# Kernel tuning notes

Measured on AMD Instinct MI355X. Metric: run time of the kernel, lower is better.

Reference implementation:

```python
import jax, jax.numpy as jnp
import numpy as np

N_NODES = 20000
N_EDGES = 320000
N_FEAT = 128
HID = 64
HEADS = 4
N_CLS = 16
NEG_SLOPE = 0.2


def setup_inputs() -> dict:
    key = jax.random.key(0)
    ks = jax.random.split(key, 12)
    x = jax.random.normal(ks[0], (N_NODES, N_FEAT), dtype=jnp.float32)
    edge_index = jax.random.randint(ks[1], (2, N_EDGES), 0, N_NODES, dtype=jnp.int64)
    # layer 1: GATConv(128 -> 64, heads=4, concat)
    s1 = 1.0 / np.sqrt(N_FEAT)
    W1 = jax.random.uniform(ks[2], (N_FEAT, HEADS * HID), jnp.float32, -s1, s1)
    a_src1 = jax.random.uniform(ks[3], (HEADS, HID), jnp.float32, -s1, s1)
    a_dst1 = jax.random.uniform(ks[4], (HEADS, HID), jnp.float32, -s1, s1)
    b1 = jnp.zeros((HEADS * HID,), jnp.float32)
    # layer 2: GATConv(256 -> 16, heads=1)
    s2 = 1.0 / np.sqrt(HEADS * HID)
    W2 = jax.random.uniform(ks[5], (HEADS * HID, N_CLS), jnp.float32, -s2, s2)
    a_src2 = jax.random.uniform(ks[6], (1, N_CLS), jnp.float32, -s2, s2)
    a_dst2 = jax.random.uniform(ks[7], (1, N_CLS), jnp.float32, -s2, s2)
    b2 = jnp.zeros((N_CLS,), jnp.float32)
    return {"x": x, "edge_index": edge_index, "W1": W1, "a_src1": a_src1,
            "a_dst1": a_dst1, "b1": b1, "W2": W2, "a_src2": a_src2,
            "a_dst2": a_dst2, "b2": b2}


def gat_conv(x, src, dst, W, a_src, a_dst, bias, n_nodes):
    # x: [N, F_in]; W: [F_in, H*C]; a_src/a_dst: [H, C]
    H, C = a_src.shape
    h = (x @ W).reshape(n_nodes, H, C)                     # [N, H, C]
    al_src = jnp.sum(h * a_src[None], axis=-1)             # [N, H]
    al_dst = jnp.sum(h * a_dst[None], axis=-1)             # [N, H]
    e = jax.nn.leaky_relu(al_src[src] + al_dst[dst], NEG_SLOPE)  # [E, H]
    # segment softmax over incoming edges of each destination node
    m = jax.ops.segment_max(e, dst, num_segments=n_nodes)  # [N, H]
    e = jnp.exp(e - m[dst])
    denom = jax.ops.segment_sum(e, dst, num_segments=n_nodes)
    alpha = e / (denom[dst] + 1e-16)                       # [E, H]
    msg = h[src] * alpha[:, :, None]                       # [E, H, C]
    out = jax.ops.segment_sum(msg, dst, num_segments=n_nodes)  # [N, H, C]
    return out.reshape(n_nodes, H * C) + bias


def reference(x, edge_index, W1, a_src1, a_dst1, b1, W2, a_src2, a_dst2, b2):
    n = x.shape[0]
    loops = jnp.arange(n, dtype=edge_index.dtype)
    src = jnp.concatenate([edge_index[0], loops])
    dst = jnp.concatenate([edge_index[1], loops])
    # eval mode: dropout is identity
    h = jax.nn.elu(gat_conv(x, src, dst, W1, a_src1, a_dst1, b1, n))
    out = gat_conv(h, src, dst, W2, a_src2, a_dst2, b2, n)
    return out
```

## Files before the change

### kernel.cpp

```cpp
#include <hip/hip_runtime.h>
#include <hip/hip_bf16.h>
#include <hip/hip_fp16.h>
#include <math.h>

#define N_NODES 20000
#define N_EDGES 320000
#define E_TOT   (N_EDGES + N_NODES)
#define N_FEAT  128
#define NEG_SLOPE 0.2f
#define MAXDEG  96

typedef _Float16 half8 __attribute__((ext_vector_type(8)));
typedef float f32x4 __attribute__((ext_vector_type(4)));

__global__ void k_zero(int* __restrict__ cur){
  int i = blockIdx.x * blockDim.x + threadIdx.x;
  if (i < N_NODES) cur[i] = 0;
}

__global__ void k_pre(const int* __restrict__ ei, int* __restrict__ cur,
                      int* __restrict__ adjS,
                      const float* __restrict__ x, _Float16* __restrict__ xh,
                      const float* __restrict__ W1, _Float16* __restrict__ W1t){
  int tid = blockIdx.x * blockDim.x + threadIdx.x;
  if (tid < E_TOT){
    int s, d;
    if (tid < N_EDGES){ s = ei[tid]; d = ei[N_EDGES + tid]; }
    else              { s = d = tid - N_EDGES; }
    int pos = atomicAdd(&cur[d], 1);
    if (pos < MAXDEG) adjS[d * MAXDEG + pos] = s;
  }
  if (tid < (N_NODES * N_FEAT / 8)){
    float4 a = *(const float4*)&x[(size_t)tid * 8];
    float4 b = *(const float4*)&x[(size_t)tid * 8 + 4];
    union { __half2 h2[4]; half8 h8; } u;
    u.h2[0] = __floats2half2_rn(a.x, a.y);
    u.h2[1] = __floats2half2_rn(a.z, a.w);
    u.h2[2] = __floats2half2_rn(b.x, b.y);
    u.h2[3] = __floats2half2_rn(b.z, b.w);
    *(half8*)&xh[(size_t)tid * 8] = u.h8;
  }
  int u2 = tid - (N_NODES * N_FEAT / 8);
  if (u2 >= 0 && u2 < 4096){
    int n = u2 >> 4, ks = u2 & 15;
    union { __half2 h2[4]; half8 h8; } u;
    float v[8];
    #pragma unroll
    for (int r = 0; r < 8; ++r) v[r] = W1[(size_t)(ks * 8 + r) * 256 + n];
    u.h2[0] = __floats2half2_rn(v[0], v[1]);
    u.h2[1] = __floats2half2_rn(v[2], v[3]);
    u.h2[2] = __floats2half2_rn(v[4], v[5]);
    u.h2[3] = __floats2half2_rn(v[6], v[7]);
    *(half8*)&W1t[(size_t)n * 128 + ks * 8] = u.h8;
  }
}

__global__ __launch_bounds__(256) void k_gemm1(
                        const _Float16* __restrict__ xh, const _Float16* __restrict__ W1t,
                        const float* __restrict__ as1, const float* __restrict__ ad1,
                        _Float16* __restrict__ h1h,
                        float* __restrict__ alS, float* __restrict__ alD){
  __shared__ _Float16 xt[64][136];
  __shared__ _Float16 Wt[64][136];
  int t  = threadIdx.x;
  int m0 = blockIdx.x * 64;
  int by = blockIdx.y;
  int j0 = by * 64;
  #pragma unroll
  for (int ii = 0; ii < 4; ++ii){
    int f = t + ii * 256;
    int r = f >> 4, s = f & 15;
    half8 xv = (half8)(_Float16)0.f;
    if (m0 + r < N_NODES) xv = *(const half8*)&xh[(size_t)(m0 + r) * 128 + s * 8];
    *(half8*)&xt[r][s * 8] = xv;
    half8 wv = *(const half8*)&W1t[(size_t)(j0 + r) * 128 + s * 8];
    *(half8*)&Wt[r][s * 8] = wv;
  }
  __syncthreads();

  int w = t >> 6, lane = t & 63;
  int g = lane >> 4, mi = lane & 15;
  f32x4 acc[4] = {};
  #pragma unroll
  for (int kk = 0; kk < 4; ++kk){
    int ko = kk * 32 + g * 8;
    half8 b = *(const half8*)&xt[w * 16 + mi][ko];
    #pragma unroll
    for (int s = 0; s < 4; ++s){
      half8 a = *(const half8*)&Wt[s * 16 + mi][ko];
      acc[s] = __builtin_amdgcn_mfma_f32_16x16x32_f16(a, b, acc[s], 0, 0, 0);
    }
  }

  int m = m0 + w * 16 + mi;
  float s_ = 0.f, d_ = 0.f;
  #pragma unroll
  for (int s = 0; s < 4; ++s){
    int nb = j0 + s * 16 + g * 4;
    float4 asv = *(const float4*)&as1[nb];
    float4 adv = *(const float4*)&ad1[nb];
    s_ += acc[s][0] * asv.x + acc[s][1] * asv.y + acc[s][2] * asv.z + acc[s][3] * asv.w;
    d_ += acc[s][0] * adv.x + acc[s][1] * adv.y + acc[s][2] * adv.z + acc[s][3] * adv.w;
    if (m < N_NODES){
      union { __half2 h2[2]; float2 f2; } u;
      u.h2[0] = __floats2half2_rn(acc[s][0], acc[s][1]);
      u.h2[1] = __floats2half2_rn(acc[s][2], acc[s][3]);
      *(float2*)&h1h[(size_t)m * 256 + nb] = u.f2;
    }
  }
  s_ += __shfl_xor(s_, 16); s_ += __shfl_xor(s_, 32);
  d_ += __shfl_xor(d_, 16); d_ += __shfl_xor(d_, 32);
  if (g == 0 && m < N_NODES){ alS[m * 4 + by] = s_; alD[m * 4 + by] = d_; }
}

__global__ __launch_bounds__(256) void k_attn1(
                        const int* __restrict__ cur, const int* __restrict__ adjS,
                        const __half* __restrict__ h1h,
                        const float* __restrict__ alS, const float* __restrict__ alD,
                        const float* __restrict__ b1, float* __restrict__ helu){
  int b    = blockIdx.x;
  int slot = b & 7;
  int h    = slot & 3;
  int g    = (slot >> 2) * 625 + (b >> 3);
  int t    = threadIdx.x;
  int w    = t >> 6, lane = t & 63;
  int grp  = lane >> 4, l16 = lane & 15;
  int n    = g * 16 + w * 4 + grp;

  int cnt  = cur[n]; cnt = (cnt > MAXDEG) ? MAXDEG : cnt;
  int start = n * MAXDEG, end = start + cnt;
  float ald = alD[n * 4 + h];
  const __half* __restrict__ hb = h1h + h * 64 + l16 * 4;

  float4 A0 = make_float4(0.f,0.f,0.f,0.f), A1 = A0, A2 = A0, A3 = A0;
  float d0 = 0.f, d1 = 0.f, d2 = 0.f, d3 = 0.f;
  int i = start;
  for (; i + 3 < end; i += 4){
    int s0 = adjS[i],     s1 = adjS[i + 1];
    int s2 = adjS[i + 2], s3 = adjS[i + 3];
    float t0 = alS[s0 * 4 + h] + ald;
    float t1 = alS[s1 * 4 + h] + ald;
    float t2 = alS[s2 * 4 + h] + ald;
    float t3 = alS[s3 * 4 + h] + ald;
    t0 = (t0 > 0.f) ? t0 : NEG_SLOPE * t0;
    t1 = (t1 > 0.f) ? t1 : NEG_SLOPE * t1;
    t2 = (t2 > 0.f) ? t2 : NEG_SLOPE * t2;
    t3 = (t3 > 0.f) ? t3 : NEG_SLOPE * t3;
    float w0 = __expf(t0), w1 = __expf(t1), w2 = __expf(t2), w3 = __expf(t3);
    float2 r0 = *(const float2*)&hb[(size_t)s0 * 256];
    float2 r1 = *(const float2*)&hb[(size_t)s1 * 256];
    float2 r2 = *(const float2*)&hb[(size_t)s2 * 256];
    float2 r3 = *(const float2*)&hb[(size_t)s3 * 256];
    const __half2* p0 = (const __half2*)&r0;
    const __half2* p1 = (const __half2*)&r1;
    const __half2* p2 = (const __half2*)&r2;
    const __half2* p3 = (const __half2*)&r3;
    float2 v0a = __half22float2(p0[0]), v0b = __half22float2(p0[1]);
    float2 v1a = __half22float2(p1[0]), v1b = __half22float2(p1[1]);
    float2 v2a = __half22float2(p2[0]), v2b = __half22float2(p2[1]);
    float2 v3a = __half22float2(p3[0]), v3b = __half22float2(p3[1]);
    A0.x += w0 * v0a.x; A0.y += w0 * v0a.y; A0.z += w0 * v0b.x; A0.w += w0 * v0b.y;
    A1.x += w1 * v1a.x; A1.y += w1 * v1a.y; A1.z += w1 * v1b.x; A1.w += w1 * v1b.y;
    A2.x += w2 * v2a.x; A2.y += w2 * v2a.y; A2.z += w2 * v2b.x; A2.w += w2 * v2b.y;
    A3.x += w3 * v3a.x; A3.y += w3 * v3a.y; A3.z += w3 * v3b.x; A3.w += w3 * v3b.y;
    d0 += w0; d1 += w1; d2 += w2; d3 += w3;
  }
  for (; i < end; ++i){
    int s0 = adjS[i];
    float t0 = alS[s0 * 4 + h] + ald;
    t0 = (t0 > 0.f) ? t0 : NEG_SLOPE * t0;
    float w0 = __expf(t0);
    float2 r0 = *(const float2*)&hb[(size_t)s0 * 256];
    const __half2* p0 = (const __half2*)&r0;
    float2 v0a = __half22float2(p0[0]), v0b = __half22float2(p0[1]);
    A0.x += w0 * v0a.x; A0.y += w0 * v0a.y; A0.z += w0 * v0b.x; A0.w += w0 * v0b.y;
    d0 += w0;
  }
  float rinv = 1.f / (((d0 + d1) + (d2 + d3)) + 1e-16f);
  float4 bv = *(const float4*)&b1[h * 64 + l16 * 4];
  float4 o;
  o.x = ((A0.x + A1.x) + (A2.x + A3.x)) * rinv + bv.x;
  o.y = ((A0.y + A1.y) + (A2.y + A3.y)) * rinv + bv.y;
  o.z = ((A0.z + A1.z) + (A2.z + A3.z)) * rinv + bv.z;
  o.w = ((A0.w + A1.w) + (A2.w + A3.w)) * rinv + bv.w;
  o.x = (o.x > 0.f) ? o.x : (__expf(o.x) - 1.f);
  o.y = (o.y > 0.f) ? o.y : (__expf(o.y) - 1.f);
  o.z = (o.z > 0.f) ? o.z : (__expf(o.z) - 1.f);
  o.w = (o.w > 0.f) ? o.w : (__expf(o.w) - 1.f);
  *(float4*)&helu[(size_t)n * 256 + h * 64 + l16 * 4] = o;
}

__global__ void k_gemm2(const float* __restrict__ helu, const float* __restrict__ W2,
                        const float* __restrict__ as2, const float* __restrict__ ad2,
                        float* __restrict__ h2, float* __restrict__ alS, float* __restrict__ alD){
  __shared__ float As[16][260];
  __shared__ float Ws[256][16];
  int t = threadIdx.x;
  int n0 = blockIdx.x * 16;
  #pragma unroll
  for (int ii = 0; ii < 4; ++ii){
    int f = t + ii * 256;
    { int r = f >> 6, c4 = f & 63;
      float4 v = *(const float4*)&helu[(size_t)(n0 + r) * 256 + c4 * 4];
      *(float4*)&As[r][c4 * 4] = v; }
    { int k = f >> 2, q = f & 3;
      float4 v = *(const float4*)&W2[(size_t)k * 16 + q * 4];
      *(float4*)&Ws[k][q * 4] = v; }
  }
  __syncthreads();
  int col = t & 15, r = t >> 4;
  float acc = 0.f;
  #pragma unroll 4
  for (int k = 0; k < 256; k += 4){
    float4 a = *(const float4*)&As[r][k];
    acc += a.x * Ws[k][col] + a.y * Ws[k + 1][col] + a.z * Ws[k + 2][col] + a.w * Ws[k + 3][col];
  }
  h2[(size_t)(n0 + r) * 16 + col] = acc;
  float s_ = acc * as2[col];
  float d_ = acc * ad2[col];
  #pragma unroll
  for (int off = 8; off; off >>= 1){ s_ += __shfl_xor(s_, off); d_ += __shfl_xor(d_, off); }
  if (col == 0){ alS[n0 + r] = s_; alD[n0 + r] = d_; }
}

__global__ __launch_bounds__(256) void k_attn2(
                        const int* __restrict__ cur, const int* __restrict__ adjS,
                        const float* __restrict__ h2,
                        const float* __restrict__ alS, const float* __restrict__ alD,
                        const float* __restrict__ b2, float* __restrict__ out){
  int t    = threadIdx.x;
  int w    = t >> 6, lane = t & 63;
  int grp  = lane >> 4, l16 = lane & 15;
  int j    = l16 >> 2, c4 = l16 & 3;
  int n    = blockIdx.x * 16 + w * 4 + grp;

  int cnt  = cur[n]; cnt = (cnt > MAXDEG) ? MAXDEG : cnt;
  int start = n * MAXDEG, end = start + cnt;
  float ald = alD[n];
  float4 acc = make_float4(0.f,0.f,0.f,0.f);
  float den = 0.f;
  for (int i = start + j; i < end; i += 4){
    int s = adjS[i];
    float tt = alS[s] + ald;
    tt = (tt > 0.f) ? tt : NEG_SLOPE * tt;
    float wv = __expf(tt);
    float4 v = *(const float4*)&h2[(size_t)s * 16 + c4 * 4];
    acc.x += wv * v.x; acc.y += wv * v.y; acc.z += wv * v.z; acc.w += wv * v.w;
    den += wv;
  }
  #pragma unroll
  for (int off = 4; off <= 8; off <<= 1){
    acc.x += __shfl_xor(acc.x, off);
    acc.y += __shfl_xor(acc.y, off);
    acc.z += __shfl_xor(acc.z, off);
    acc.w += __shfl_xor(acc.w, off);
    den   += __shfl_xor(den, off);
  }
  if (j == 0){
    float rinv = 1.f / (den + 1e-16f);
    float4 bv = *(const float4*)&b2[c4 * 4];
    float4 o;
    o.x = acc.x * rinv + bv.x; o.y = acc.y * rinv + bv.y;
    o.z = acc.z * rinv + bv.z; o.w = acc.w * rinv + bv.w;
    *(float4*)&out[(size_t)n * 16 + c4 * 4] = o;
  }
}

extern "C" void kernel_launch(void* const* d_in, const int* in_sizes, int n_in,
                              void* d_out, int out_size, void* d_ws, size_t ws_size,
                              hipStream_t stream){
  const float* x   = (const float*)d_in[0];
  const int*   ei  = (const int*)d_in[1];
  const float* W1  = (const float*)d_in[2];
  const float* as1 = (const float*)d_in[3];
  const float* ad1 = (const float*)d_in[4];
  const float* b1  = (const float*)d_in[5];
  const float* W2  = (const float*)d_in[6];
  const float* as2 = (const float*)d_in[7];
  const float* ad2 = (const float*)d_in[8];
  const float* b2  = (const float*)d_in[9];
  float* out = (float*)d_out;

  float* fws = (float*)d_ws;
  size_t off = 0;
  __half* h1h = (__half*)(fws + off); off += (size_t)N_NODES * 128;
  _Float16* xh  = (_Float16*)(fws + off); off += (size_t)N_NODES * 64;
  _Float16* W1t = (_Float16*)(fws + off); off += 256 * 64;
  float* helu = fws + off; off += (size_t)N_NODES * 256;
  float* h2   = fws + off; off += (size_t)N_NODES * 16;
  float* alS1 = fws + off; off += N_NODES * 4;
  float* alD1 = fws + off; off += N_NODES * 4;
  float* alS2 = fws + off; off += N_NODES;
  float* alD2 = fws + off; off += N_NODES;
  int* cur  = (int*)(fws + off); off += N_NODES;
  int* adjS = (int*)(fws + off); off += (size_t)N_NODES * MAXDEG;

  const int XW = N_NODES * N_FEAT / 8 + 4096;
  const int PRE_N = (E_TOT > XW ? E_TOT : XW);

  k_zero<<<(N_NODES + 255) / 256, 256, 0, stream>>>(cur);
  k_pre<<<(PRE_N + 255) / 256, 256, 0, stream>>>(ei, cur, adjS, x, xh, W1, W1t);
  k_gemm1<<<dim3(313, 4), 256, 0, stream>>>(xh, W1t, as1, ad1, (_Float16*)h1h, alS1, alD1);
  k_attn1<<<5000, 256, 0, stream>>>(cur, adjS, h1h, alS1, alD1, b1, helu);
  k_gemm2<<<1250, 256, 0, stream>>>(helu, W2, as2, ad2, h2, alS2, alD2);
  k_attn2<<<1250, 256, 0, stream>>>(cur, adjS, h2, alS2, alD2, b2, out);
}
```

Baseline: 89.92 us.

## Store layer-1 output in fp16 and compute second GEMM with MFMA

```diff
diff --git a/kernel.cpp b/kernel.cpp
--- a/kernel.cpp
+++ b/kernel.cpp
@@ -117,7 +117,7 @@
                         const int* __restrict__ cur, const int* __restrict__ adjS,
                         const __half* __restrict__ h1h,
                         const float* __restrict__ alS, const float* __restrict__ alD,
-                        const float* __restrict__ b1, float* __restrict__ helu){
+                        const float* __restrict__ b1, _Float16* __restrict__ heluh){
   int b    = blockIdx.x;
   int slot = b & 7;
   int h    = slot & 3;
@@ -132,95 +132,118 @@
   float ald = alD[n * 4 + h];
   const __half* __restrict__ hb = h1h + h * 64 + l16 * 4;
 
-  float4 A0 = make_float4(0.f,0.f,0.f,0.f), A1 = A0, A2 = A0, A3 = A0;
-  float d0 = 0.f, d1 = 0.f, d2 = 0.f, d3 = 0.f;
+  float4 A[8]; float dn[8];
+  #pragma unroll
+  for (int q = 0; q < 8; ++q){ A[q] = make_float4(0.f,0.f,0.f,0.f); dn[q] = 0.f; }
+
   int i = start;
-  for (; i + 3 < end; i += 4){
-    int s0 = adjS[i],     s1 = adjS[i + 1];
-    int s2 = adjS[i + 2], s3 = adjS[i + 3];
-    float t0 = alS[s0 * 4 + h] + ald;
-    float t1 = alS[s1 * 4 + h] + ald;
-    float t2 = alS[s2 * 4 + h] + ald;
-    float t3 = alS[s3 * 4 + h] + ald;
-    t0 = (t0 > 0.f) ? t0 : NEG_SLOPE * t0;
-    t1 = (t1 > 0.f) ? t1 : NEG_SLOPE * t1;
-    t2 = (t2 > 0.f) ? t2 : NEG_SLOPE * t2;
-    t3 = (t3 > 0.f) ? t3 : NEG_SLOPE * t3;
-    float w0 = __expf(t0), w1 = __expf(t1), w2 = __expf(t2), w3 = __expf(t3);
-    float2 r0 = *(const float2*)&hb[(size_t)s0 * 256];
-    float2 r1 = *(const float2*)&hb[(size_t)s1 * 256];
-    float2 r2 = *(const float2*)&hb[(size_t)s2 * 256];
-    float2 r3 = *(const float2*)&hb[(size_t)s3 * 256];
-    const __half2* p0 = (const __half2*)&r0;
-    const __half2* p1 = (const __half2*)&r1;
-    const __half2* p2 = (const __half2*)&r2;
-    const __half2* p3 = (const __half2*)&r3;
-    float2 v0a = __half22float2(p0[0]), v0b = __half22float2(p0[1]);
-    float2 v1a = __half22float2(p1[0]), v1b = __half22float2(p1[1]);
-    float2 v2a = __half22float2(p2[0]), v2b = __half22float2(p2[1]);
-    float2 v3a = __half22float2(p3[0]), v3b = __half22float2(p3[1]);
-    A0.x += w0 * v0a.x; A0.y += w0 * v0a.y; A0.z += w0 * v0b.x; A0.w += w0 * v0b.y;
-    A1.x += w1 * v1a.x; A1.y += w1 * v1a.y; A1.z += w1 * v1b.x; A1.w += w1 * v1b.y;
-    A2.x += w2 * v2a.x; A2.y += w2 * v2a.y; A2.z += w2 * v2b.x; A2.w += w2 * v2b.y;
-    A3.x += w3 * v3a.x; A3.y += w3 * v3a.y; A3.z += w3 * v3b.x; A3.w += w3 * v3b.y;
-    d0 += w0; d1 += w1; d2 += w2; d3 += w3;
+  for (; i + 7 < end; i += 8){
+    int ss[8]; float ww[8];
+    #pragma unroll
+    for (int q = 0; q < 8; ++q) ss[q] = adjS[i + q];
+    #pragma unroll
+    for (int q = 0; q < 8; ++q){
+      float tt = alS[ss[q] * 4 + h] + ald;
+      tt = (tt > 0.f) ? tt : NEG_SLOPE * tt;
+      ww[q] = __expf(tt);
+    }
+    #pragma unroll
+    for (int q = 0; q < 8; ++q){
+      float2 rr = *(const float2*)&hb[(size_t)ss[q] * 256];
+      const __half2* pp = (const __half2*)&rr;
+      float2 va = __half22float2(pp[0]), vb = __half22float2(pp[1]);
+      A[q].x += ww[q] * va.x; A[q].y += ww[q] * va.y;
+      A[q].z += ww[q] * vb.x; A[q].w += ww[q] * vb.y;
+      dn[q] += ww[q];
+    }
   }
   for (; i < end; ++i){
     int s0 = adjS[i];
-    float t0 = alS[s0 * 4 + h] + ald;
-    t0 = (t0 > 0.f) ? t0 : NEG_SLOPE * t0;
-    float w0 = __expf(t0);
-    float2 r0 = *(const float2*)&hb[(size_t)s0 * 256];
-    const __half2* p0 = (const __half2*)&r0;
-    float2 v0a = __half22float2(p0[0]), v0b = __half22float2(p0[1]);
-    A0.x += w0 * v0a.x; A0.y += w0 * v0a.y; A0.z += w0 * v0b.x; A0.w += w0 * v0b.y;
-    d0 += w0;
-  }
-  float rinv = 1.f / (((d0 + d1) + (d2 + d3)) + 1e-16f);
+    float tt = alS[s0 * 4 + h] + ald;
+    tt = (tt > 0.f) ? tt : NEG_SLOPE * tt;
+    float w0 = __expf(tt);
+    float2 rr = *(const float2*)&hb[(size_t)s0 * 256];
+    const __half2* pp = (const __half2*)&rr;
+    float2 va = __half22float2(pp[0]), vb = __half22float2(pp[1]);
+    A[0].x += w0 * va.x; A[0].y += w0 * va.y; A[0].z += w0 * vb.x; A[0].w += w0 * vb.y;
+    dn[0] += w0;
+  }
+  #pragma unroll
+  for (int q = 4; q > 0; q >>= 1)
+    #pragma unroll
+    for (int p = 0; p < q; ++p){
+      A[p].x += A[p + q].x; A[p].y += A[p + q].y;
+      A[p].z += A[p + q].z; A[p].w += A[p + q].w;
+      dn[p] += dn[p + q];
+    }
+  float rinv = 1.f / (dn[0] + 1e-16f);
   float4 bv = *(const float4*)&b1[h * 64 + l16 * 4];
   float4 o;
-  o.x = ((A0.x + A1.x) + (A2.x + A3.x)) * rinv + bv.x;
-  o.y = ((A0.y + A1.y) + (A2.y + A3.y)) * rinv + bv.y;
-  o.z = ((A0.z + A1.z) + (A2.z + A3.z)) * rinv + bv.z;
-  o.w = ((A0.w + A1.w) + (A2.w + A3.w)) * rinv + bv.w;
+  o.x = A[0].x * rinv + bv.x;
+  o.y = A[0].y * rinv + bv.y;
+  o.z = A[0].z * rinv + bv.z;
+  o.w = A[0].w * rinv + bv.w;
   o.x = (o.x > 0.f) ? o.x : (__expf(o.x) - 1.f);
   o.y = (o.y > 0.f) ? o.y : (__expf(o.y) - 1.f);
   o.z = (o.z > 0.f) ? o.z : (__expf(o.z) - 1.f);
   o.w = (o.w > 0.f) ? o.w : (__expf(o.w) - 1.f);
-  *(float4*)&helu[(size_t)n * 256 + h * 64 + l16 * 4] = o;
-}
-
-__global__ void k_gemm2(const float* __restrict__ helu, const float* __restrict__ W2,
+  union { __half2 h2[2]; float2 f2; } u;
+  u.h2[0] = __floats2half2_rn(o.x, o.y);
+  u.h2[1] = __floats2half2_rn(o.z, o.w);
+  *(float2*)&heluh[(size_t)n * 256 + h * 64 + l16 * 4] = u.f2;
+}
+
+__global__ __launch_bounds__(256) void k_gemm2(
+                        const _Float16* __restrict__ heluh, const float* __restrict__ W2,
                         const float* __restrict__ as2, const float* __restrict__ ad2,
                         float* __restrict__ h2, float* __restrict__ alS, float* __restrict__ alD){
-  __shared__ float As[16][260];
-  __shared__ float Ws[256][16];
+  __shared__ _Float16 Ht[64][264];
+  __shared__ _Float16 Wt[16][264];
   int t = threadIdx.x;
-  int n0 = blockIdx.x * 16;
-  #pragma unroll
-  for (int ii = 0; ii < 4; ++ii){
+  int n0 = blockIdx.x * 64;
+  #pragma unroll
+  for (int ii = 0; ii < 8; ++ii){
     int f = t + ii * 256;
-    { int r = f >> 6, c4 = f & 63;
-      float4 v = *(const float4*)&helu[(size_t)(n0 + r) * 256 + c4 * 4];
-      *(float4*)&As[r][c4 * 4] = v; }
-    { int k = f >> 2, q = f & 3;
-      float4 v = *(const float4*)&W2[(size_t)k * 16 + q * 4];
-      *(float4*)&Ws[k][q * 4] = v; }
+    int r = f >> 5, s = f & 31;
+    half8 v = (half8)(_Float16)0.f;
+    if (n0 + r < N_NODES) v = *(const half8*)&heluh[(size_t)(n0 + r) * 256 + s * 8];
+    *(half8*)&Ht[r][s * 8] = v;
+  }
+  {
+    int k = t;
+    float4 w0 = *(const float4*)&W2[k * 16 + 0];
+    float4 w1 = *(const float4*)&W2[k * 16 + 4];
+    float4 w2 = *(const float4*)&W2[k * 16 + 8];
+    float4 w3 = *(const float4*)&W2[k * 16 + 12];
+    float wv[16] = {w0.x,w0.y,w0.z,w0.w, w1.x,w1.y,w1.z,w1.w,
+                    w2.x,w2.y,w2.z,w2.w, w3.x,w3.y,w3.z,w3.w};
+    #pragma unroll
+    for (int c = 0; c < 16; ++c) Wt[c][k] = (_Float16)wv[c];
   }
   __syncthreads();
-  int col = t & 15, r = t >> 4;
-  float acc = 0.f;
-  #pragma unroll 4
-  for (int k = 0; k < 256; k += 4){
-    float4 a = *(const float4*)&As[r][k];
-    acc += a.x * Ws[k][col] + a.y * Ws[k + 1][col] + a.z * Ws[k + 2][col] + a.w * Ws[k + 3][col];
-  }
-  h2[(size_t)(n0 + r) * 16 + col] = acc;
-  float s_ = acc * as2[col];
-  float d_ = acc * ad2[col];
-  #pragma unroll
-  for (int off = 8; off; off >>= 1){ s_ += __shfl_xor(s_, off); d_ += __shfl_xor(d_, off); }
-  if (col == 0){ alS[n0 + r] = s_; alD[n0 + r] = d_; }
+
+  int w = t >> 6, lane = t & 63;
+  int g = lane >> 4, mi = lane & 15;
+  f32x4 acc = {};
+  #pragma unroll
+  for (int kk = 0; kk < 8; ++kk){
+    int ko = kk * 32 + g * 8;
+    half8 b = *(const half8*)&Ht[w * 16 + mi][ko];
+    half8 a = *(const half8*)&Wt[mi][ko];
+    acc = __builtin_amdgcn_mfma_f32_16x16x32_f16(a, b, acc, 0, 0, 0);
+  }
+  int n = n0 + w * 16 + mi;
+  float4 asv = *(const float4*)&as2[g * 4];
+  float4 adv = *(const float4*)&ad2[g * 4];
+  float s_ = acc[0] * asv.x + acc[1] * asv.y + acc[2] * asv.z + acc[3] * asv.w;
+  float d_ = acc[0] * adv.x + acc[1] * adv.y + acc[2] * adv.z + acc[3] * adv.w;
+  s_ += __shfl_xor(s_, 16); s_ += __shfl_xor(s_, 32);
+  d_ += __shfl_xor(d_, 16); d_ += __shfl_xor(d_, 32);
+  if (n < N_NODES){
+    float4 hv = make_float4(acc[0], acc[1], acc[2], acc[3]);
+    *(float4*)&h2[(size_t)n * 16 + g * 4] = hv;
+    if (g == 0){ alS[n] = s_; alD[n] = d_; }
+  }
 }
 
 __global__ __launch_bounds__(256) void k_attn2(
@@ -286,7 +309,7 @@
   __half* h1h = (__half*)(fws + off); off += (size_t)N_NODES * 128;
   _Float16* xh  = (_Float16*)(fws + off); off += (size_t)N_NODES * 64;
   _Float16* W1t = (_Float16*)(fws + off); off += 256 * 64;
-  float* helu = fws + off; off += (size_t)N_NODES * 256;
+  _Float16* heluh = (_Float16*)(fws + off); off += (size_t)N_NODES * 128;
   float* h2   = fws + off; off += (size_t)N_NODES * 16;
   float* alS1 = fws + off; off += N_NODES * 4;
   float* alD1 = fws + off; off += N_NODES * 4;
@@ -301,7 +324,7 @@
   k_zero<<<(N_NODES + 255) / 256, 256, 0, stream>>>(cur);
   k_pre<<<(PRE_N + 255) / 256, 256, 0, stream>>>(ei, cur, adjS, x, xh, W1, W1t);
   k_gemm1<<<dim3(313, 4), 256, 0, stream>>>(xh, W1t, as1, ad1, (_Float16*)h1h, alS1, alD1);
-  k_attn1<<<5000, 256, 0, stream>>>(cur, adjS, h1h, alS1, alD1, b1, helu);
-  k_gemm2<<<1250, 256, 0, stream>>>(helu, W2, as2, ad2, h2, alS2, alD2);
+  k_attn1<<<5000, 256, 0, stream>>>(cur, adjS, h1h, alS1, alD1, b1, heluh);
+  k_gemm2<<<313, 256, 0, stream>>>(heluh, W2, as2, ad2, h2, alS2, alD2);
   k_attn2<<<1250, 256, 0, stream>>>(cur, adjS, h2, alS2, alD2, b2, out);
 }
```

Result: slower. 102.1 us (+13.5%).

## Store layer-1 ELU output in fp16 and compute layer-2 GEMM with MFMA

Applied to the files above, without the earlier changes.

```diff
diff --git a/kernel.cpp b/kernel.cpp
--- a/kernel.cpp
+++ b/kernel.cpp
@@ -117,7 +117,7 @@
                         const int* __restrict__ cur, const int* __restrict__ adjS,
                         const __half* __restrict__ h1h,
                         const float* __restrict__ alS, const float* __restrict__ alD,
-                        const float* __restrict__ b1, float* __restrict__ helu){
+                        const float* __restrict__ b1, _Float16* __restrict__ heluh){
   int b    = blockIdx.x;
   int slot = b & 7;
   int h    = slot & 3;
@@ -187,40 +187,63 @@
   o.y = (o.y > 0.f) ? o.y : (__expf(o.y) - 1.f);
   o.z = (o.z > 0.f) ? o.z : (__expf(o.z) - 1.f);
   o.w = (o.w > 0.f) ? o.w : (__expf(o.w) - 1.f);
-  *(float4*)&helu[(size_t)n * 256 + h * 64 + l16 * 4] = o;
-}
-
-__global__ void k_gemm2(const float* __restrict__ helu, const float* __restrict__ W2,
+  union { __half2 h2[2]; float2 f2; } u;
+  u.h2[0] = __floats2half2_rn(o.x, o.y);
+  u.h2[1] = __floats2half2_rn(o.z, o.w);
+  *(float2*)&heluh[(size_t)n * 256 + h * 64 + l16 * 4] = u.f2;
+}
+
+__global__ __launch_bounds__(256) void k_gemm2(
+                        const _Float16* __restrict__ heluh, const float* __restrict__ W2,
                         const float* __restrict__ as2, const float* __restrict__ ad2,
                         float* __restrict__ h2, float* __restrict__ alS, float* __restrict__ alD){
-  __shared__ float As[16][260];
-  __shared__ float Ws[256][16];
+  __shared__ _Float16 Ht[64][264];
+  __shared__ _Float16 Wt[16][264];
   int t = threadIdx.x;
-  int n0 = blockIdx.x * 16;
-  #pragma unroll
-  for (int ii = 0; ii < 4; ++ii){
+  int n0 = blockIdx.x * 64;
+  #pragma unroll
+  for (int ii = 0; ii < 8; ++ii){
     int f = t + ii * 256;
-    { int r = f >> 6, c4 = f & 63;
-      float4 v = *(const float4*)&helu[(size_t)(n0 + r) * 256 + c4 * 4];
-      *(float4*)&As[r][c4 * 4] = v; }
-    { int k = f >> 2, q = f & 3;
-      float4 v = *(const float4*)&W2[(size_t)k * 16 + q * 4];
-      *(float4*)&Ws[k][q * 4] = v; }
+    int r = f >> 5, s = f & 31;
+    half8 v = (half8)(_Float16)0.f;
+    if (n0 + r < N_NODES) v = *(const half8*)&heluh[(size_t)(n0 + r) * 256 + s * 8];
+    *(half8*)&Ht[r][s * 8] = v;
+  }
+  {
+    int k = t;
+    float4 w0 = *(const float4*)&W2[k * 16 + 0];
+    float4 w1 = *(const float4*)&W2[k * 16 + 4];
+    float4 w2 = *(const float4*)&W2[k * 16 + 8];
+    float4 w3 = *(const float4*)&W2[k * 16 + 12];
+    float wv[16] = {w0.x,w0.y,w0.z,w0.w, w1.x,w1.y,w1.z,w1.w,
+                    w2.x,w2.y,w2.z,w2.w, w3.x,w3.y,w3.z,w3.w};
+    #pragma unroll
+    for (int c = 0; c < 16; ++c) Wt[c][k] = (_Float16)wv[c];
   }
   __syncthreads();
-  int col = t & 15, r = t >> 4;
-  float acc = 0.f;
-  #pragma unroll 4
-  for (int k = 0; k < 256; k += 4){
-    float4 a = *(const float4*)&As[r][k];
-    acc += a.x * Ws[k][col] + a.y * Ws[k + 1][col] + a.z * Ws[k + 2][col] + a.w * Ws[k + 3][col];
-  }
-  h2[(size_t)(n0 + r) * 16 + col] = acc;
-  float s_ = acc * as2[col];
-  float d_ = acc * ad2[col];
-  #pragma unroll
-  for (int off = 8; off; off >>= 1){ s_ += __shfl_xor(s_, off); d_ += __shfl_xor(d_, off); }
-  if (col == 0){ alS[n0 + r] = s_; alD[n0 + r] = d_; }
+
+  int w = t >> 6, lane = t & 63;
+  int g = lane >> 4, mi = lane & 15;
+  f32x4 acc = {};
+  #pragma unroll
+  for (int kk = 0; kk < 8; ++kk){
+    int ko = kk * 32 + g * 8;
+    half8 b = *(const half8*)&Ht[w * 16 + mi][ko];
+    half8 a = *(const half8*)&Wt[mi][ko];
+    acc = __builtin_amdgcn_mfma_f32_16x16x32_f16(a, b, acc, 0, 0, 0);
+  }
+  int n = n0 + w * 16 + mi;
+  float4 asv = *(const float4*)&as2[g * 4];
+  float4 adv = *(const float4*)&ad2[g * 4];
+  float s_ = acc[0] * asv.x + acc[1] * asv.y + acc[2] * asv.z + acc[3] * asv.w;
+  float d_ = acc[0] * adv.x + acc[1] * adv.y + acc[2] * adv.z + acc[3] * adv.w;
+  s_ += __shfl_xor(s_, 16); s_ += __shfl_xor(s_, 32);
+  d_ += __shfl_xor(d_, 16); d_ += __shfl_xor(d_, 32);
+  if (n < N_NODES){
+    float4 hv = make_float4(acc[0], acc[1], acc[2], acc[3]);
+    *(float4*)&h2[(size_t)n * 16 + g * 4] = hv;
+    if (g == 0){ alS[n] = s_; alD[n] = d_; }
+  }
 }
 
 __global__ __launch_bounds__(256) void k_attn2(
@@ -286,7 +309,7 @@
   __half* h1h = (__half*)(fws + off); off += (size_t)N_NODES * 128;
   _Float16* xh  = (_Float16*)(fws + off); off += (size_t)N_NODES * 64;
   _Float16* W1t = (_Float16*)(fws + off); off += 256 * 64;
-  float* helu = fws + off; off += (size_t)N_NODES * 256;
+  _Float16* heluh = (_Float16*)(fws + off); off += (size_t)N_NODES * 128;
   float* h2   = fws + off; off += (size_t)N_NODES * 16;
   float* alS1 = fws + off; off += N_NODES * 4;
   float* alD1 = fws + off; off += N_NODES * 4;
@@ -301,7 +324,7 @@
   k_zero<<<(N_NODES + 255) / 256, 256, 0, stream>>>(cur);
   k_pre<<<(PRE_N + 255) / 256, 256, 0, stream>>>(ei, cur, adjS, x, xh, W1, W1t);
   k_gemm1<<<dim3(313, 4), 256, 0, stream>>>(xh, W1t, as1, ad1, (_Float16*)h1h, alS1, alD1);
-  k_attn1<<<5000, 256, 0, stream>>>(cur, adjS, h1h, alS1, alD1, b1, helu);
-  k_gemm2<<<1250, 256, 0, stream>>>(helu, W2, as2, ad2, h2, alS2, alD2);
+  k_attn1<<<5000, 256, 0, stream>>>(cur, adjS, h1h, alS1, alD1, b1, heluh);
+  k_gemm2<<<313, 256, 0, stream>>>(heluh, W2, as2, ad2, h2, alS2, alD2);
   k_attn2<<<1250, 256, 0, stream>>>(cur, adjS, h2, alS2, alD2, b2, out);
 }
```

New measurement: 91.12 us. Within noise of the previous version (+1.3%).
